# Performance work log

Hardware: AMD Instinct MI355X
Metric: run time of the kernel (lower is better)

## Reference

```python
import jax, jax.numpy as jnp
import numpy as np

N = 100000      # n_nodes
D = 128         # n_features
H = 64          # n_filters (hidden)
C = 40          # n_classes
NNZ = 3200000   # n_edges (avg degree 32)


def setup_inputs() -> dict:
    key = jax.random.key(0)
    ks = jax.random.split(key, 6)
    x = jax.random.normal(ks[0], (N, D), dtype=jnp.float32)
    edge_idx = jax.random.randint(ks[1], (2, NNZ), 0, N, dtype=jnp.int32)
    edge_weight = jnp.ones((NNZ,), dtype=jnp.float32)
    # Glorot-ish init for linear weights
    W1 = jax.random.normal(ks[2], (D, H), dtype=jnp.float32) / np.sqrt(D)
    b1 = jnp.zeros((H,), dtype=jnp.float32)
    W2 = jax.random.normal(ks[3], (H, C), dtype=jnp.float32) / np.sqrt(H)
    b2 = jnp.zeros((C,), dtype=jnp.float32)
    return {"x": x, "edge_idx": edge_idx, "edge_weight": edge_weight,
            "W1": W1, "b1": b1, "W2": W2, "b2": b2}


def gcn_norm(edge_idx, edge_weight, n):
    """PyG gcn_norm: add self-loops (weight 1), symmetric D^-1/2 A D^-1/2."""
    loop = jnp.arange(n, dtype=edge_idx.dtype)
    row = jnp.concatenate([edge_idx[0], loop])  # source
    col = jnp.concatenate([edge_idx[1], loop])  # target
    w = jnp.concatenate([edge_weight, jnp.ones((n,), edge_weight.dtype)])
    deg = jax.ops.segment_sum(w, col, num_segments=n)
    dis = jnp.where(deg > 0, jax.lax.rsqrt(deg), 0.0)
    norm = dis[row] * w * dis[col]
    return row, col, norm


def gcn_conv(h, row, col, norm, W, b):
    # linear transform then sparse aggregation: out[col] += norm * (h @ W)[row]
    h = h @ W
    out = jax.ops.segment_sum(h[row] * norm[:, None], col, num_segments=h.shape[0])
    return out + b


def reference(x, edge_idx, edge_weight, W1, b1, W2, b2):
    n = x.shape[0]
    # adjacency normalized once and cached (do_normalize_adj_once=True)
    row, col, norm = gcn_norm(edge_idx, edge_weight, n)
    h = gcn_conv(x, row, col, norm, W1, b1)
    h = jax.nn.relu(h)
    # dropout is identity at inference time
    out = gcn_conv(h, row, col, norm, W2, b2)
    return out
```

## Files before the change

kernel.cpp:

```cpp
#include <hip/hip_runtime.h>
#include <hip/hip_bf16.h>
#include <cstdint>

#define NN   100000
#define DD   128
#define HH   64
#define CC   40
#define NNZE 3200000


__global__ void k_zero(int* cnt, int n) {
    int i = blockIdx.x * blockDim.x + threadIdx.x;
    if (i < n) cnt[i] = 0;
}

__global__ void k_count(const int* __restrict__ col, int* cnt, int* rank, int nnz4) {
    int i = blockIdx.x * blockDim.x + threadIdx.x;
    if (i < nnz4) {
        int4 c = ((const int4*)col)[i];
        int r0 = atomicAdd(&cnt[c.x], 1);
        int r1 = atomicAdd(&cnt[c.y], 1);
        int r2 = atomicAdd(&cnt[c.z], 1);
        int r3 = atomicAdd(&cnt[c.w], 1);
        ((int4*)rank)[i] = make_int4(r0, r1, r2, r3);
    }
}


__global__ void scan_k1(const int* __restrict__ cnt, int* offs, int* bsum, int n) {
    __shared__ int s[256];
    int t = threadIdx.x, b = blockIdx.x;
    int base = b * 1024 + t * 4;
    int v0 = (base + 0 < n) ? cnt[base + 0] : 0;
    int v1 = (base + 1 < n) ? cnt[base + 1] : 0;
    int v2 = (base + 2 < n) ? cnt[base + 2] : 0;
    int v3 = (base + 3 < n) ? cnt[base + 3] : 0;
    int tsum = v0 + v1 + v2 + v3;
    s[t] = tsum;
    __syncthreads();
    for (int off = 1; off < 256; off <<= 1) {
        int x = (t >= off) ? s[t - off] : 0;
        __syncthreads();
        s[t] += x;
        __syncthreads();
    }
    int incl = s[t];
    int p = incl - tsum;
    if (base + 0 < n) offs[base + 0] = p; p += v0;
    if (base + 1 < n) offs[base + 1] = p; p += v1;
    if (base + 2 < n) offs[base + 2] = p; p += v2;
    if (base + 3 < n) offs[base + 3] = p;
    if (t == 255) bsum[b] = incl;
}

__global__ void scan_k2(int* bsum, int nb, int* offs, int n) {
    if (threadIdx.x == 0 && blockIdx.x == 0) {
        int run = 0;
        for (int i = 0; i < nb; i++) { int v = bsum[i]; bsum[i] = run; run += v; }
        offs[n] = run;
    }
}

__global__ void scan_k3(int* offs, const int* __restrict__ bsum, int n) {
    int i = blockIdx.x * blockDim.x + threadIdx.x;
    if (i < n) offs[i] += bsum[i >> 10];
}


__global__ void k_fill(const int* __restrict__ row, const int* __restrict__ col,
                       const float* __restrict__ w, const int* __restrict__ rank,
                       const int* __restrict__ offs,
                       int2* __restrict__ csr, int nnz4) {
    int i = blockIdx.x * blockDim.x + threadIdx.x;
    if (i < nnz4) {
        int4   r  = ((const int4*)row)[i];
        int4   c  = ((const int4*)col)[i];
        int4   rk = ((const int4*)rank)[i];
        float4 wv = ((const float4*)w)[i];
        csr[offs[c.x] + rk.x] = make_int2(r.x, __float_as_int(wv.x));
        csr[offs[c.y] + rk.y] = make_int2(r.y, __float_as_int(wv.y));
        csr[offs[c.z] + rk.z] = make_int2(r.z, __float_as_int(wv.z));
        csr[offs[c.w] + rk.w] = make_int2(r.w, __float_as_int(wv.w));
    }
}


__global__ void k_degdis(const int* __restrict__ offs, const int2* __restrict__ csr,
                         float* dis, int n) {
    int i = blockIdx.x * blockDim.x + threadIdx.x;
    if (i < n) {
        float s = 1.0f;
        int e0 = offs[i], e1 = offs[i + 1];
        for (int j = e0; j < e1; j++) s += __int_as_float(csr[j].y);
        dis[i] = s > 0.f ? rsqrtf(s) : 0.f;
    }
}


__global__ __launch_bounds__(256) void k_gemm1(const float* __restrict__ x,
                                               const float* __restrict__ W1,
                                               float* __restrict__ h1, int n) {
    __shared__ float ws[128 * 64];
    __shared__ float xs[16 * 129];
    int t = threadIdx.x;
    for (int i = t; i < 128 * 64; i += 256) ws[i] = W1[i];
    int row0 = blockIdx.x * 64;
    int r = t >> 4, cg = t & 15;
    for (int p = 0; p < 4; p++) {
        __syncthreads();
        int rbase = row0 + p * 16;
        for (int i = t; i < 512; i += 256) {
            int li = i * 4;
            int rr = li >> 7, kk = li & 127;
            float4 v = make_float4(0.f, 0.f, 0.f, 0.f);
            if (rbase + rr < n) v = *(const float4*)&x[(rbase + rr) * 128 + kk];
            xs[rr * 129 + kk + 0] = v.x;
            xs[rr * 129 + kk + 1] = v.y;
            xs[rr * 129 + kk + 2] = v.z;
            xs[rr * 129 + kk + 3] = v.w;
        }
        __syncthreads();
        float4 acc = make_float4(0.f, 0.f, 0.f, 0.f);
        for (int k = 0; k < 128; k++) {
            float xa = xs[r * 129 + k];
            float4 w4 = *(const float4*)&ws[k * 64 + cg * 4];
            acc.x += xa * w4.x; acc.y += xa * w4.y;
            acc.z += xa * w4.z; acc.w += xa * w4.w;
        }
        int rowi = rbase + r;
        if (rowi < n) *(float4*)&h1[rowi * 64 + cg * 4] = acc;
    }
}


__global__ __launch_bounds__(256) void k_agg1(const float* __restrict__ h1,
                                              const int* __restrict__ offs,
                                              const int2* __restrict__ csr,
                                              const float* __restrict__ dis,
                                              const float* __restrict__ b1,
                                              const float* __restrict__ W2,
                                              float* __restrict__ g, int n) {
    __shared__ float w2s[64 * 40];
    __shared__ float sh2[4][64];
    __shared__ int   ssrc[4][64];
    __shared__ float sa[4][64];
    int t = threadIdx.x;
    for (int i = t; i < 64 * 40; i += 256) w2s[i] = W2[i];
    __syncthreads();
    int w = t >> 6, l = t & 63;
    int c = blockIdx.x * 4 + w;
    if (c >= n) return;
    float dc = dis[c];
    float selfh = h1[c * 64 + l];
    float acc = 0.f;
    int start = offs[c], end = offs[c + 1];
    for (int base = start; base < end; base += 64) {
        int m = end - base; if (m > 64) m = 64;
        if (l < m) {
            int2 pk = csr[base + l];
            ssrc[w][l] = pk.x;
            sa[w][l] = __int_as_float(pk.y) * dis[pk.x];
        }
        for (int j = 0; j < m; j++) {
            acc += sa[w][j] * h1[ssrc[w][j] * 64 + l];
        }
    }
    float hv = dc * acc + dc * dc * selfh + b1[l];
    hv = hv > 0.f ? hv : 0.f;
    sh2[w][l] = hv;
    if (l < 40) {
        float gv = 0.f;
        for (int k = 0; k < 64; k++) gv += sh2[w][k] * w2s[k * 40 + l];
        g[c * 40 + l] = gv;
    }
}


__global__ __launch_bounds__(256) void k_agg2(const float* __restrict__ g,
                                              const int* __restrict__ offs,
                                              const int2* __restrict__ csr,
                                              const float* __restrict__ dis,
                                              const float* __restrict__ b2,
                                              float* __restrict__ out, int n) {
    __shared__ int   ssrc[4][64];
    __shared__ float sa[4][64];
    int t = threadIdx.x;
    int w = t >> 6, l = t & 63;
    int c = blockIdx.x * 4 + w;
    if (c >= n) return;
    float dc = dis[c];
    float acc = 0.f;
    int start = offs[c], end = offs[c + 1];
    for (int base = start; base < end; base += 64) {
        int m = end - base; if (m > 64) m = 64;
        if (l < m) {
            int2 pk = csr[base + l];
            ssrc[w][l] = pk.x;
            sa[w][l] = __int_as_float(pk.y) * dis[pk.x];
        }
        if (l < 40) {
            for (int j = 0; j < m; j++) {
                acc += sa[w][j] * g[ssrc[w][j] * 40 + l];
            }
        }
    }
    if (l < 40) {
        float selfg = g[c * 40 + l];
        out[c * 40 + l] = dc * acc + dc * dc * selfg + b2[l];
    }
}


extern "C" void kernel_launch(void* const* d_in, const int* in_sizes, int n_in,
                              void* d_out, int out_size, void* d_ws, size_t ws_size,
                              hipStream_t stream) {
    const float* x  = (const float*)d_in[0];
    const int*   ei = (const int*)d_in[1];
    const float* ew = (const float*)d_in[2];
    const float* W1 = (const float*)d_in[3];
    const float* b1 = (const float*)d_in[4];
    const float* W2 = (const float*)d_in[5];
    const float* b2 = (const float*)d_in[6];
    float* out = (float*)d_out;

    const int n = NN, nnz = NNZE;
    const int* erow = ei;
    const int* ecol = ei + nnz;

    char* p = (char*)d_ws;
    auto alloc = [&](size_t bytes) {
        void* r = (void*)p;
        p += (bytes + 255) & ~(size_t)255;
        return r;
    };
    float* dis  = (float*)alloc((size_t)n * 4);
    int*   offs = (int*)  alloc((size_t)(n + 1) * 4);
    int*   cnt  = (int*)  alloc((size_t)n * 4);
    int*   bsum = (int*)  alloc((size_t)128 * 4);
    int2*  csr  = (int2*) alloc((size_t)nnz * 8);
    float* h1   = (float*)alloc((size_t)n * HH * 4);
    float* g    = (float*)alloc((size_t)n * CC * 4);
    int*   rank = (int*)h1;
    (void)ws_size;

    const int NB_N  = (n + 255) / 256;
    const int NB_E4 = (nnz / 4 + 255) / 256;
    const int NB_SC = (n + 1023) / 1024;

    k_zero  <<<NB_N, 256, 0, stream>>>(cnt, n);
    k_count <<<NB_E4, 256, 0, stream>>>(ecol, cnt, rank, nnz / 4);
    scan_k1 <<<NB_SC, 256, 0, stream>>>(cnt, offs, bsum, n);
    scan_k2 <<<1, 64, 0, stream>>>(bsum, NB_SC, offs, n);
    scan_k3 <<<NB_N, 256, 0, stream>>>(offs, bsum, n);
    k_fill  <<<NB_E4, 256, 0, stream>>>(erow, ecol, ew, rank, offs, csr, nnz / 4);
    k_degdis<<<NB_N, 256, 0, stream>>>(offs, csr, dis, n);
    k_gemm1 <<<(n + 63) / 64, 256, 0, stream>>>(x, W1, h1, n);
    k_agg1  <<<(n + 3) / 4, 256, 0, stream>>>(h1, offs, csr, dis, b1, W2, g, n);
    k_agg2  <<<(n + 3) / 4, 256, 0, stream>>>(g, offs, csr, dis, b2, out, n);
}
```

Before: 629.9 us.

## Store intermediates in fp16, fuse count with GEMM1, parallelize block scan

Stores the hidden features h1 and the second-layer features g as fp16 instead of fp32, halving the bytes moved by the two random-gather aggregations. GEMM1 is merged into the edge-count kernel as extra blocks, so the atomic counting and the dense GEMM can run concurrently; the GEMM now reads x straight from global memory instead of staging it in shared memory. The single-thread block-sum scan becomes a parallel shared-memory scan. g is pre-scaled by the source's inverse square-root degree, which removes the dis[src] gather in the second aggregation. The cost is reduced precision in the intermediates, plus a separate rank buffer because h1 can no longer be aliased.

```diff
diff --git a/kernel.cpp b/kernel.cpp
--- a/kernel.cpp
+++ b/kernel.cpp
@@ -1,5 +1,6 @@
 #include <hip/hip_runtime.h>
 #include <hip/hip_bf16.h>
+#include <hip/hip_fp16.h>
 #include <cstdint>
 
 #define NN   100000
@@ -14,15 +15,47 @@
     if (i < n) cnt[i] = 0;
 }
 
-__global__ void k_count(const int* __restrict__ col, int* cnt, int* rank, int nnz4) {
-    int i = blockIdx.x * blockDim.x + threadIdx.x;
-    if (i < nnz4) {
-        int4 c = ((const int4*)col)[i];
-        int r0 = atomicAdd(&cnt[c.x], 1);
-        int r1 = atomicAdd(&cnt[c.y], 1);
-        int r2 = atomicAdd(&cnt[c.z], 1);
-        int r3 = atomicAdd(&cnt[c.w], 1);
-        ((int4*)rank)[i] = make_int4(r0, r1, r2, r3);
+
+__global__ __launch_bounds__(256) void k_count_gemm(
+        const int* __restrict__ col, int* cnt, int* rank, int nnz4,
+        const float* __restrict__ x, const float* __restrict__ W1,
+        __half* __restrict__ h1h, int n, int nCB) {
+    __shared__ float ws[128 * 64];
+    int bid = blockIdx.x, t = threadIdx.x;
+    if (bid < nCB) {
+        int i = bid * 256 + t;
+        if (i < nnz4) {
+            int4 c = ((const int4*)col)[i];
+            int r0 = atomicAdd(&cnt[c.x], 1);
+            int r1 = atomicAdd(&cnt[c.y], 1);
+            int r2 = atomicAdd(&cnt[c.z], 1);
+            int r3 = atomicAdd(&cnt[c.w], 1);
+            ((int4*)rank)[i] = make_int4(r0, r1, r2, r3);
+        }
+        return;
+    }
+    int gb = bid - nCB;
+    for (int i = t; i < 128 * 64; i += 256) ws[i] = W1[i];
+    __syncthreads();
+    int row0 = gb * 64;
+    int r = t >> 4, cg = t & 15;
+    for (int p = 0; p < 4; p++) {
+        int rowi = row0 + p * 16 + r;
+        if (rowi < n) {
+            const float* xrow = x + (size_t)rowi * 128;
+            float4 acc = make_float4(0.f, 0.f, 0.f, 0.f);
+            #pragma unroll 8
+            for (int k = 0; k < 128; k++) {
+                float xa = xrow[k];
+                float4 w4 = *(const float4*)&ws[k * 64 + cg * 4];
+                acc.x += xa * w4.x; acc.y += xa * w4.y;
+                acc.z += xa * w4.z; acc.w += xa * w4.w;
+            }
+            __half2 lo = __floats2half2_rn(acc.x, acc.y);
+            __half2 hi = __floats2half2_rn(acc.z, acc.w);
+            *(__half2*)&h1h[rowi * 64 + cg * 4 + 0] = lo;
+            *(__half2*)&h1h[rowi * 64 + cg * 4 + 2] = hi;
+        }
     }
 }
 
@@ -53,12 +86,20 @@
     if (t == 255) bsum[b] = incl;
 }
 
-__global__ void scan_k2(int* bsum, int nb, int* offs, int n) {
-    if (threadIdx.x == 0 && blockIdx.x == 0) {
-        int run = 0;
-        for (int i = 0; i < nb; i++) { int v = bsum[i]; bsum[i] = run; run += v; }
-        offs[n] = run;
-    }
+__global__ void scan_k2p(int* bsum, int nb, int* offs, int n) {
+    __shared__ int s[128];
+    int t = threadIdx.x;
+    int v = (t < nb) ? bsum[t] : 0;
+    s[t] = v;
+    __syncthreads();
+    for (int off = 1; off < 128; off <<= 1) {
+        int x = (t >= off) ? s[t - off] : 0;
+        __syncthreads();
+        s[t] += x;
+        __syncthreads();
+    }
+    if (t < nb) bsum[t] = s[t] - v;
+    if (t == 127) offs[n] = s[127];
 }
 
 __global__ void scan_k3(int* offs, const int* __restrict__ bsum, int n) {
@@ -97,49 +138,13 @@
 }
 
 
-__global__ __launch_bounds__(256) void k_gemm1(const float* __restrict__ x,
-                                               const float* __restrict__ W1,
-                                               float* __restrict__ h1, int n) {
-    __shared__ float ws[128 * 64];
-    __shared__ float xs[16 * 129];
-    int t = threadIdx.x;
-    for (int i = t; i < 128 * 64; i += 256) ws[i] = W1[i];
-    int row0 = blockIdx.x * 64;
-    int r = t >> 4, cg = t & 15;
-    for (int p = 0; p < 4; p++) {
-        __syncthreads();
-        int rbase = row0 + p * 16;
-        for (int i = t; i < 512; i += 256) {
-            int li = i * 4;
-            int rr = li >> 7, kk = li & 127;
-            float4 v = make_float4(0.f, 0.f, 0.f, 0.f);
-            if (rbase + rr < n) v = *(const float4*)&x[(rbase + rr) * 128 + kk];
-            xs[rr * 129 + kk + 0] = v.x;
-            xs[rr * 129 + kk + 1] = v.y;
-            xs[rr * 129 + kk + 2] = v.z;
-            xs[rr * 129 + kk + 3] = v.w;
-        }
-        __syncthreads();
-        float4 acc = make_float4(0.f, 0.f, 0.f, 0.f);
-        for (int k = 0; k < 128; k++) {
-            float xa = xs[r * 129 + k];
-            float4 w4 = *(const float4*)&ws[k * 64 + cg * 4];
-            acc.x += xa * w4.x; acc.y += xa * w4.y;
-            acc.z += xa * w4.z; acc.w += xa * w4.w;
-        }
-        int rowi = rbase + r;
-        if (rowi < n) *(float4*)&h1[rowi * 64 + cg * 4] = acc;
-    }
-}
-
-
-__global__ __launch_bounds__(256) void k_agg1(const float* __restrict__ h1,
+__global__ __launch_bounds__(256) void k_agg1(const __half* __restrict__ h1h,
                                               const int* __restrict__ offs,
                                               const int2* __restrict__ csr,
                                               const float* __restrict__ dis,
                                               const float* __restrict__ b1,
                                               const float* __restrict__ W2,
-                                              float* __restrict__ g, int n) {
+                                              __half* __restrict__ gh, int n) {
     __shared__ float w2s[64 * 40];
     __shared__ float sh2[4][64];
     __shared__ int   ssrc[4][64];
@@ -151,7 +156,7 @@
     int c = blockIdx.x * 4 + w;
     if (c >= n) return;
     float dc = dis[c];
-    float selfh = h1[c * 64 + l];
+    float selfh = __half2float(h1h[c * 64 + l]);
     float acc = 0.f;
     int start = offs[c], end = offs[c + 1];
     for (int base = start; base < end; base += 64) {
@@ -162,7 +167,7 @@
             sa[w][l] = __int_as_float(pk.y) * dis[pk.x];
         }
         for (int j = 0; j < m; j++) {
-            acc += sa[w][j] * h1[ssrc[w][j] * 64 + l];
+            acc += sa[w][j] * __half2float(h1h[ssrc[w][j] * 64 + l]);
         }
     }
     float hv = dc * acc + dc * dc * selfh + b1[l];
@@ -171,12 +176,12 @@
     if (l < 40) {
         float gv = 0.f;
         for (int k = 0; k < 64; k++) gv += sh2[w][k] * w2s[k * 40 + l];
-        g[c * 40 + l] = gv;
-    }
-}
-
-
-__global__ __launch_bounds__(256) void k_agg2(const float* __restrict__ g,
+        gh[c * 40 + l] = __float2half_rn(gv * dc);
+    }
+}
+
+
+__global__ __launch_bounds__(256) void k_agg2(const __half* __restrict__ gh,
                                               const int* __restrict__ offs,
                                               const int2* __restrict__ csr,
                                               const float* __restrict__ dis,
@@ -196,17 +201,17 @@
         if (l < m) {
             int2 pk = csr[base + l];
             ssrc[w][l] = pk.x;
-            sa[w][l] = __int_as_float(pk.y) * dis[pk.x];
+            sa[w][l] = __int_as_float(pk.y);
         }
         if (l < 40) {
             for (int j = 0; j < m; j++) {
-                acc += sa[w][j] * g[ssrc[w][j] * 40 + l];
+                acc += sa[w][j] * __half2float(gh[ssrc[w][j] * 40 + l]);
             }
         }
     }
     if (l < 40) {
-        float selfg = g[c * 40 + l];
-        out[c * 40 + l] = dc * acc + dc * dc * selfg + b2[l];
+        float selfgs = __half2float(gh[c * 40 + l]);
+        out[c * 40 + l] = dc * (acc + selfgs) + b2[l];
     }
 }
 
@@ -233,28 +238,29 @@
         p += (bytes + 255) & ~(size_t)255;
         return r;
     };
-    float* dis  = (float*)alloc((size_t)n * 4);
-    int*   offs = (int*)  alloc((size_t)(n + 1) * 4);
-    int*   cnt  = (int*)  alloc((size_t)n * 4);
-    int*   bsum = (int*)  alloc((size_t)128 * 4);
-    int2*  csr  = (int2*) alloc((size_t)nnz * 8);
-    float* h1   = (float*)alloc((size_t)n * HH * 4);
-    float* g    = (float*)alloc((size_t)n * CC * 4);
-    int*   rank = (int*)h1;
+    float*  dis  = (float*)alloc((size_t)n * 4);
+    int*    offs = (int*)  alloc((size_t)(n + 1) * 4);
+    int*    cnt  = (int*)  alloc((size_t)n * 4);
+    int*    bsum = (int*)  alloc((size_t)128 * 4);
+    int2*   csr  = (int2*) alloc((size_t)nnz * 8);
+    int*    rank = (int*)  alloc((size_t)nnz * 4);
+    __half* h1h  = (__half*)alloc((size_t)n * HH * 2);
+    __half* gh   = (__half*)alloc((size_t)n * CC * 2);
     (void)ws_size;
 
     const int NB_N  = (n + 255) / 256;
     const int NB_E4 = (nnz / 4 + 255) / 256;
+    const int NB_G  = (n + 63) / 64;
     const int NB_SC = (n + 1023) / 1024;
 
-    k_zero  <<<NB_N, 256, 0, stream>>>(cnt, n);
-    k_count <<<NB_E4, 256, 0, stream>>>(ecol, cnt, rank, nnz / 4);
-    scan_k1 <<<NB_SC, 256, 0, stream>>>(cnt, offs, bsum, n);
-    scan_k2 <<<1, 64, 0, stream>>>(bsum, NB_SC, offs, n);
-    scan_k3 <<<NB_N, 256, 0, stream>>>(offs, bsum, n);
-    k_fill  <<<NB_E4, 256, 0, stream>>>(erow, ecol, ew, rank, offs, csr, nnz / 4);
-    k_degdis<<<NB_N, 256, 0, stream>>>(offs, csr, dis, n);
-    k_gemm1 <<<(n + 63) / 64, 256, 0, stream>>>(x, W1, h1, n);
-    k_agg1  <<<(n + 3) / 4, 256, 0, stream>>>(h1, offs, csr, dis, b1, W2, g, n);
-    k_agg2  <<<(n + 3) / 4, 256, 0, stream>>>(g, offs, csr, dis, b2, out, n);
-}
+    k_zero      <<<NB_N, 256, 0, stream>>>(cnt, n);
+    k_count_gemm<<<NB_E4 + NB_G, 256, 0, stream>>>(ecol, cnt, rank, nnz / 4,
+                                                   x, W1, h1h, n, NB_E4);
+    scan_k1     <<<NB_SC, 256, 0, stream>>>(cnt, offs, bsum, n);
+    scan_k2p    <<<1, 128, 0, stream>>>(bsum, NB_SC, offs, n);
+    scan_k3     <<<NB_N, 256, 0, stream>>>(offs, bsum, n);
+    k_fill      <<<NB_E4, 256, 0, stream>>>(erow, ecol, ew, rank, offs, csr, nnz / 4);
+    k_degdis    <<<NB_N, 256, 0, stream>>>(offs, csr, dis, n);
+    k_agg1      <<<(n + 3) / 4, 256, 0, stream>>>(h1h, offs, csr, dis, b1, W2, gh, n);
+    k_agg2      <<<(n + 3) / 4, 256, 0, stream>>>(gh, offs, csr, dis, b2, out, n);
+}
```

New measurement: 567.3 us. 9.9% less time.
